# Kernel optimization log

Hardware: AMD Instinct MI355X
Metric: run time of the kernel (lower is better)

## Reference

```python
import jax, jax.numpy as jnp
import numpy as np
from functools import partial

B, EMB, H, V, T = 128, 512, 1024, 8192, 100
START_VALUE = 0


def setup_inputs() -> dict:
    key = jax.random.key(0)
    ks = jax.random.split(key, 8)
    s = 0.05
    return {
        "x": jax.random.normal(ks[0], (B, H), jnp.float32),
        "emb_table": jax.random.normal(ks[1], (V, EMB), jnp.float32) * s,
        "w_ih": jax.random.normal(ks[2], (3 * H, EMB), jnp.float32) * s,
        "w_hh": jax.random.normal(ks[3], (3 * H, H), jnp.float32) * s,
        "b_ih": jax.random.normal(ks[4], (3 * H,), jnp.float32) * s,
        "b_hh": jax.random.normal(ks[5], (3 * H,), jnp.float32) * s,
        "cls_w": jax.random.normal(ks[6], (V, H), jnp.float32) * s,
        "cls_b": jax.random.normal(ks[7], (V,), jnp.float32) * s,
    }


def _gru_cell(e, h, w_ih, w_hh, b_ih, b_hh):
    # PyTorch GRU cell math. e: [B,EMB], h: [B,H]
    gi = e @ w_ih.T + b_ih  # [B, 3H]
    gh = h @ w_hh.T + b_hh  # [B, 3H]
    i_r, i_z, i_n = jnp.split(gi, 3, axis=1)
    h_r, h_z, h_n = jnp.split(gh, 3, axis=1)
    r = jax.nn.sigmoid(i_r + h_r)
    z = jax.nn.sigmoid(i_z + h_z)
    n = jnp.tanh(i_n + r * h_n)
    return (1.0 - z) * n + z * h


def reference(x, emb_table, w_ih, w_hh, b_ih, b_hh, cls_w, cls_b):
    # start distribution: log_softmax of one-hot at START_VALUE
    start_val = jax.nn.log_softmax(
        jnp.zeros((V,), x.dtype).at[START_VALUE].set(1.0), axis=0
    )
    prev0 = jnp.broadcast_to(start_val, (B, V))

    def step(carry, _):
        h, prev_logp = carry
        idx = jnp.argmax(prev_logp, axis=1)          # [B]
        e = emb_table[idx]                           # [B, EMB]
        h_new = _gru_cell(e, h, w_ih, w_hh, b_ih, b_hh)
        logp = jax.nn.log_softmax(h_new @ cls_w.T + cls_b, axis=1)  # [B, V]
        return (h_new, logp), logp

    _, outs = jax.lax.scan(step, (x, prev0), None, length=T - 1)
    outs = jnp.transpose(outs, (1, 0, 2))            # [B, T-1, V]
    return jnp.concatenate([prev0[:, None, :], outs], axis=1)  # [B, T, V]
```

## Files before the change

kernel.cpp:

```cpp
#include <hip/hip_runtime.h>
#include <stdint.h>


#define Bb   128
#define EMBd 512
#define Hd   1024
#define Vd   8192
#define Td   100
#define HPB  524288

typedef __attribute__((ext_vector_type(8))) _Float16 half8;
typedef __attribute__((ext_vector_type(4))) float f32x4;
typedef unsigned long long ull;

#define LOSCALE 2048.0f
#define LOINV   (1.0f/2048.0f)

#define WAITV(N) do { asm volatile("s_waitcnt vmcnt(" #N ")" ::: "memory"); \
                      __builtin_amdgcn_sched_barrier(0); } while (0)
#define WAITL    do { asm volatile("s_waitcnt lgkmcnt(0)" ::: "memory");    \
                      __builtin_amdgcn_sched_barrier(0); } while (0)

__device__ __forceinline__ uint32_t fkey(float f) {
  uint32_t u = __float_as_uint(f);
  return (u & 0x80000000u) ? ~u : (u | 0x80000000u);
}
__device__ __forceinline__ ull umax64(ull a, ull b) { return a > b ? a : b; }

__device__ __forceinline__ void dma16(const void* g, void* l) {
  __builtin_amdgcn_global_load_lds((const uint32_t*)g, (uint32_t*)l, 16, 0, 0);
}
__device__ __forceinline__ void st16sc(void* p, half8 v) {
  f32x4 d = *(f32x4*)&v;
  asm volatile("global_store_dwordx4 %0, %1, off sc0 sc1"
               :: "v"(p), "v"(d) : "memory");
}
__device__ __forceinline__ ull sysld64(const ull* p) {
  return __hip_atomic_load((ull*)p, __ATOMIC_RELAXED, __HIP_MEMORY_SCOPE_SYSTEM);
}
__device__ __forceinline__ uint32_t ld32sys(uint32_t* p) {
  return __hip_atomic_load(p, __ATOMIC_RELAXED, __HIP_MEMORY_SCOPE_SYSTEM);
}
__device__ __forceinline__ void st32sys(uint32_t* p, uint32_t v) {
  __hip_atomic_store(p, v, __ATOMIC_RELAXED, __HIP_MEMORY_SCOPE_SYSTEM);
}
__device__ __forceinline__ uint32_t add32sys(uint32_t* p, uint32_t v) {
  return __hip_atomic_fetch_add(p, v, __ATOMIC_RELAXED, __HIP_MEMORY_SCOPE_SYSTEM);
}

__device__ __forceinline__ void cvt8(const float4 v0, const float4 v1,
                                     half8& hh, half8& ll) {
  float vv[8] = {v0.x, v0.y, v0.z, v0.w, v1.x, v1.y, v1.z, v1.w};
#pragma unroll
  for (int i = 0; i < 8; ++i) {
    _Float16 h = (_Float16)vv[i];
    hh[i] = h;
    ll[i] = (_Float16)((vv[i] - (float)h) * LOSCALE);
  }
}

__global__ void k_init(const float* __restrict__ x, float* __restrict__ hbuf0,
                       ull* __restrict__ amax, char* __restrict__ hpre0,
                       uint32_t* __restrict__ bar) {
  int tid = blockIdx.x * 256 + threadIdx.x;
  if (tid < Bb * Hd) hbuf0[tid] = x[tid];
  if (tid < Td * Bb) amax[tid] = (tid < Bb) ? 0xFFFFFFFFull : 0ull;
  if (tid >= 16384 && tid < 16640)
    bar[tid - 16384] = (tid - 16384 == 8) ? 128u : 0u;
  if (tid < 16384) {
    int b = tid & 127, sc = tid >> 7;
    int st = sc >> 2, c = sc & 3;
    const float* src = x + b * Hd + st * 32 + c * 8;
    float4 v0 = *(const float4*)src, v1 = *(const float4*)(src + 4);
    half8 hh, ll; cvt8(v0, v1, hh, ll);
    char* hp = hpre0 + st * 16384 + b * 128;
    *(half8*)(hp + ((c       ^ (b & 7))) * 16) = hh;
    *(half8*)(hp + (((c + 4) ^ (b & 7))) * 16) = ll;
  }
}

__global__ void k_prep_emb(const float* __restrict__ emb, char* __restrict__ embp) {
  int t = blockIdx.x * 256 + threadIdx.x;
  int row = t >> 6, rem = t & 63, st = rem >> 2, c = rem & 3;
  const float* src = emb + (size_t)row * EMBd + st * 32 + c * 8;
  float4 v0 = *(const float4*)src, v1 = *(const float4*)(src + 4);
  half8 hh, ll; cvt8(v0, v1, hh, ll);
  char* d = embp + (size_t)row * 2048 + st * 128;
  *(half8*)(d + c * 16) = hh;
  *(half8*)(d + (c + 4) * 16) = ll;
}

__global__ void k_prep_w(const float* __restrict__ w_ih, const float* __restrict__ w_hh,
                         char* __restrict__ wpre) {
  int bi = blockIdx.x;
  int st = bi % 12, t2 = bi / 12, q = t2 & 3, cg = t2 >> 2;
  int t = threadIdx.x; if (t >= 192) return;
  int r = t >> 2, c = t & 3;
  int g = r >> 4, bn = r & 15;
  int k0 = q * 384 + st * 32 + c * 8;
  const float* src = (k0 < 512)
    ? (w_ih + (size_t)(g * 1024 + cg * 16 + bn) * EMBd + k0)
    : (w_hh + (size_t)(g * 1024 + cg * 16 + bn) * Hd + (k0 - 512));
  float4 v0 = *(const float4*)src, v1 = *(const float4*)(src + 4);
  half8 hh, ll; cvt8(v0, v1, hh, ll);
  char* d = wpre + (size_t)bi * 6144 + r * 128;
  *(half8*)(d + ((c       ^ (r & 7))) * 16) = hh;
  *(half8*)(d + (((c + 4) ^ (r & 7))) * 16) = ll;
}

__global__ void k_prep_cls(const float* __restrict__ cls_w, char* __restrict__ clsp) {
  int b = blockIdx.x;
  int ct = b >> 5, st = b & 31;
  int t = threadIdx.x;
  int r = t >> 2, c = t & 3;
  const float* src = cls_w + (size_t)(ct * 64 + r) * Hd + st * 32 + c * 8;
  float4 v0 = *(const float4*)src, v1 = *(const float4*)(src + 4);
  half8 hh, ll; cvt8(v0, v1, hh, ll);
  char* d = clsp + (size_t)b * 8192 + r * 128;
  *(half8*)(d + ((c       ^ (r & 7))) * 16) = hh;
  *(half8*)(d + (((c + 4) ^ (r & 7))) * 16) = ll;
}

__global__ __launch_bounds__(256, 2) void k_prep_gi(
    const char* __restrict__ embp, const char* __restrict__ wpre,
    const float* __restrict__ b_ih, float* __restrict__ gi)
{
  const int cg = blockIdx.x, vh = blockIdx.y;
  const int tid = threadIdx.x, lane = tid & 63, w = tid >> 6;
  const int C = cg * 16;
  __shared__ __align__(16) char pA[4 * 8192];
  __shared__ __align__(16) char pB[4 * 6144];

  f32x4 accH[3], accL[3];
#pragma unroll
  for (int g = 0; g < 3; ++g) {
    accH[g] = (f32x4){0.f, 0.f, 0.f, 0.f};
    accL[g] = (f32x4){0.f, 0.f, 0.f, 0.f};
  }

  const int rr = lane >> 3, cc = lane & 7;
  const char* abase = embp + (size_t)(vh * 64 + w * 16 + rr) * 2048 + ((cc ^ rr) * 16);

  auto issue = [&](int st) {
    char* da = pA + (st & 3) * 8192 + w * 2048;
    const char* s0 = abase + st * 128;
    dma16(s0, da);
    dma16(s0 + 8 * 2048, da + 1024);
    const int wq = st / 12, wst = st - wq * 12;
    const char* sb = wpre + (size_t)((cg * 4 + wq) * 12 + wst) * 6144 + w * 1536 + lane * 16;
    char* db = pB + (st & 3) * 6144 + w * 1536;
    dma16(sb, db);
    if (lane < 32) dma16(sb + 1024, db + 1024);
  };

  const int l15 = lane & 15, qd = lane >> 4, r7 = l15 & 7;
  const int offAH = (w * 16 + l15) * 128 + ((qd)     ^ r7) * 16;
  const int offAL = (w * 16 + l15) * 128 + ((qd + 4) ^ r7) * 16;

  issue(0); issue(1); issue(2);
  WAITV(8);
  __builtin_amdgcn_s_barrier();

  for (int st = 0; st < 16; ++st) {
    const int bf = st & 3;
    half8 aH = *(half8*)&pA[bf * 8192 + offAH];
    half8 aL = *(half8*)&pA[bf * 8192 + offAL];
    if (st + 3 < 16) issue(st + 3);
#pragma unroll
    for (int g = 0; g < 3; ++g) {
      half8 bH = *(half8*)&pB[bf * 6144 + (g * 16 + l15) * 128 + ((qd)     ^ r7) * 16];
      half8 bL = *(half8*)&pB[bf * 6144 + (g * 16 + l15) * 128 + ((qd + 4) ^ r7) * 16];
      accH[g] = __builtin_amdgcn_mfma_f32_16x16x32_f16(aH, bH, accH[g], 0, 0, 0);
      accL[g] = __builtin_amdgcn_mfma_f32_16x16x32_f16(aH, bL, accL[g], 0, 0, 0);
      accL[g] = __builtin_amdgcn_mfma_f32_16x16x32_f16(aL, bH, accL[g], 0, 0, 0);
    }
    if (st < 15) {
      if (st <= 12)      { WAITV(8); }
      else if (st == 13) { WAITV(4); }
      else               { WAITV(0); }
      WAITL;
      __builtin_amdgcn_s_barrier();
    }
  }

  const int v0 = vh * 64 + w * 16 + qd * 4;
#pragma unroll
  for (int g = 0; g < 3; ++g) {
    float bi = b_ih[g * 1024 + C + l15];
#pragma unroll
    for (int i = 0; i < 4; ++i) {
      float val = accH[g][i] + accL[g][i] * LOINV + bi;
      gi[(size_t)(v0 + i) * 3072 + g * 1024 + C + l15] = val;
    }
  }
}

__global__ __launch_bounds__(256) void k_loop(
    const char* __restrict__ wpre, const char* __restrict__ clsp,
    const float* __restrict__ gi,
    const float* __restrict__ b_hh, const float* __restrict__ cls_b,
    float* __restrict__ hbuf, char* __restrict__ hpre,
    ull* __restrict__ amax, float* __restrict__ out,
    uint32_t* __restrict__ bar)
{
  const int wg = blockIdx.x;
  const int tid = threadIdx.x, lane = tid & 63, w = tid >> 6;
  __shared__ __align__(16) char smem[98304];

  if (tid == 0)
    (void)__hip_atomic_load(&bar[200], __ATOMIC_ACQUIRE, __HIP_MEMORY_SCOPE_AGENT);
  __syncthreads();

  uint32_t* gCnt   = &bar[0];
  uint32_t* hReady = &bar[1];
  uint32_t* aCnt   = &bar[8];

  const int l15 = lane & 15, qd = lane >> 4, r7 = l15 & 7;
  const int offA_H = (w * 16 + l15) * 128 + ((qd)     ^ r7) * 16;
  const int offA_L = (w * 16 + l15) * 128 + ((qd + 4) ^ r7) * 16;

  if (wg < 128) {
    const int cg = wg & 63, rh = wg >> 6;
    const int C = cg * 16;
    char* gA = smem;
    char* gB = smem + 32768;

    for (int s = 1; s < Td; ++s) {
      if (tid == 0)
        while (ld32sys(hReady) < (uint32_t)(s - 1)) __builtin_amdgcn_s_sleep(2);
      __syncthreads();

      const char* hsrc = hpre + (size_t)(s - 1) * HPB + rh * 8192 + w * 2048 + lane * 16;

      f32x4 accH[3], accL[3];
#pragma unroll
      for (int g = 0; g < 3; ++g) {
        accH[g] = (f32x4){0.f, 0.f, 0.f, 0.f};
        accL[g] = (f32x4){0.f, 0.f, 0.f, 0.f};
      }

      auto issue = [&](int st) {
        char* da = gA + (st & 3) * 8192 + w * 2048;
        const char* sa = hsrc + st * 16384;
        dma16(sa, da);
        dma16(sa + 1024, da + 1024);
        const int k0 = 512 + st * 32;
        const int wq = (k0 >= 1152) ? 3 : (k0 >= 768 ? 2 : 1);
        const int wst = (k0 - wq * 384) >> 5;
        const char* sb = wpre + (size_t)((cg * 4 + wq) * 12 + wst) * 6144 + w * 1536 + lane * 16;
        char* db = gB + (st & 3) * 6144 + w * 1536;
        dma16(sb, db);
        if (lane < 32) dma16(sb + 1024, db + 1024);
      };

      issue(0); issue(1); issue(2);
      WAITV(8);
      __builtin_amdgcn_s_barrier();

      for (int st = 0; st < 32; ++st) {
        const int bf = st & 3;
        half8 aH = *(half8*)&gA[bf * 8192 + offA_H];
        half8 aL = *(half8*)&gA[bf * 8192 + offA_L];
        if (st + 3 < 32) issue(st + 3);
#pragma unroll
        for (int g = 0; g < 3; ++g) {
          half8 bH = *(half8*)&gB[bf * 6144 + (g * 16 + l15) * 128 + ((qd)     ^ r7) * 16];
          half8 bL = *(half8*)&gB[bf * 6144 + (g * 16 + l15) * 128 + ((qd + 4) ^ r7) * 16];
          accH[g] = __builtin_amdgcn_mfma_f32_16x16x32_f16(aH, bH, accH[g], 0, 0, 0);
          accL[g] = __builtin_amdgcn_mfma_f32_16x16x32_f16(aH, bL, accL[g], 0, 0, 0);
          accL[g] = __builtin_amdgcn_mfma_f32_16x16x32_f16(aL, bH, accL[g], 0, 0, 0);
        }
        if (st < 31) {
          if (st <= 28)      { WAITV(8); }
          else if (st == 29) { WAITV(4); }
          else               { WAITV(0); }
          WAITL;
          __builtin_amdgcn_s_barrier();
        }
      }

      if (tid == 0)
        while (ld32sys(&aCnt[s - 1]) < 128u) __builtin_amdgcn_s_sleep(2);
      __syncthreads();

      const int j = C + l15;
      const float bh0 = b_hh[j], bh1 = b_hh[1024 + j], bh2 = b_hh[2048 + j];
      const float* hprev_f = hbuf + (size_t)((s - 1) & 1) * Bb * Hd;
      float* hnew_f = hbuf + (size_t)(s & 1) * Bb * Hd;
      const ull* amax_prev = amax + (size_t)(s - 1) * Bb;
      float outs[4];
#pragma unroll
      for (int i = 0; i < 4; ++i) {
        const int ri = rh * 64 + w * 16 + qd * 4 + i;
        const uint32_t idx = (~(uint32_t)sysld64(&amax_prev[ri])) & 8191u;
        const float* gp = gi + (size_t)idx * 3072 + j;
        float i_r = gp[0], i_z = gp[1024], i_n = gp[2048];
        float h_r = accH[0][i] + accL[0][i] * LOINV + bh0;
        float h_z = accH[1][i] + accL[1][i] * LOINV + bh1;
        float h_n = accH[2][i] + accL[2][i] * LOINV + bh2;
        float rr2 = 1.f / (1.f + expf(-(i_r + h_r)));
        float zz = 1.f / (1.f + expf(-(i_z + h_z)));
        float nn = tanhf(i_n + rr2 * h_n);
        float o = (1.f - zz) * nn + zz * hprev_f[ri * Hd + j];
        hnew_f[ri * Hd + j] = o;
        outs[i] = o;
      }
      __syncthreads();
      float* sT = (float*)smem;
#pragma unroll
      for (int i = 0; i < 4; ++i)
        sT[(w * 16 + qd * 4 + i) * 16 + l15] = outs[i];
      __syncthreads();
      if (tid < 128) {
        const int row = tid >> 1, half = tid & 1;
        const int b = rh * 64 + row;
        const float* srcp = sT + row * 16 + half * 8;
        half8 hh, ll;
#pragma unroll
        for (int e = 0; e < 8; ++e) {
          float o = srcp[e];
          _Float16 oh = (_Float16)o;
          hh[e] = oh;
          ll[e] = (_Float16)((o - (float)oh) * LOSCALE);
        }
        const int stp = C >> 5;
        const int chb = ((C & 31) >> 3) + half;
        char* hp = hpre + (size_t)s * HPB + stp * 16384 + b * 128;
        st16sc(hp + ((chb       ^ (b & 7))) * 16, hh);
        st16sc(hp + (((chb + 4) ^ (b & 7))) * 16, ll);
      }
      WAITV(0);
      __syncthreads();
      if (tid == 0) {
        uint32_t old = add32sys(gCnt, 1u);
        if (old + 1u == 128u * (uint32_t)s)
          st32sys(hReady, (uint32_t)s);
      }
    }
  } else {
    const int wgC = wg - 128;
    const int ct2 = wgC & 63, rt0 = wgC >> 6;
    const int r0c = rt0 * 64;
    char* cA = smem;
    char* cB = smem + 32768;
    const char* bb0 = clsp + (size_t)(2 * ct2)     * 262144 + w * 2048 + lane * 16;
    const char* bb1 = clsp + (size_t)(2 * ct2 + 1) * 262144 + w * 2048 + lane * 16;

    for (int s = 1; s < Td; ++s) {
      if (tid == 0)
        while (ld32sys(hReady) < (uint32_t)s) __builtin_amdgcn_s_sleep(2);
      __syncthreads();

      const char* asrc = hpre + (size_t)s * HPB + rt0 * 8192 + w * 2048 + lane * 16;

      f32x4 accH[8], accL[8];
#pragma unroll
      for (int i = 0; i < 8; ++i) {
        accH[i] = (f32x4){0.f, 0.f, 0.f, 0.f};
        accL[i] = (f32x4){0.f, 0.f, 0.f, 0.f};
      }

      auto issue = [&](int st) {
        char* da = cA + (st & 3) * 8192 + w * 2048;
        const char* sa = asrc + st * 16384;
        dma16(sa, da);
        dma16(sa + 1024, da + 1024);
        char* db = cB + (st & 3) * 16384 + w * 2048;
        const char* s0 = bb0 + st * 8192;
        dma16(s0, db);
        dma16(s0 + 1024, db + 1024);
        const char* s1 = bb1 + st * 8192;
        dma16(s1, db + 8192);
        dma16(s1 + 1024, db + 8192 + 1024);
      };

      issue(0); issue(1); issue(2);
      WAITV(12);
      __builtin_amdgcn_s_barrier();

      for (int st = 0; st < 32; ++st) {
        const int bf = st & 3;
        half8 aH = *(half8*)&cA[bf * 8192 + offA_H];
        half8 aL = *(half8*)&cA[bf * 8192 + offA_L];
        if (st + 3 < 32) issue(st + 3);
#pragma unroll
        for (int cf = 0; cf < 8; ++cf) {
          const int bo = bf * 16384 + (cf >> 2) * 8192 + ((cf & 3) * 16 + l15) * 128;
          half8 bH = *(half8*)&cB[bo + ((qd)     ^ r7) * 16];
          half8 bL = *(half8*)&cB[bo + ((qd + 4) ^ r7) * 16];
          accH[cf] = __builtin_amdgcn_mfma_f32_16x16x32_f16(aH, bH, accH[cf], 0, 0, 0);
          accL[cf] = __builtin_amdgcn_mfma_f32_16x16x32_f16(aH, bL, accL[cf], 0, 0, 0);
          accL[cf] = __builtin_amdgcn_mfma_f32_16x16x32_f16(aL, bH, accL[cf], 0, 0, 0);
        }
        if (st < 31) {
          if (st <= 28)      { WAITV(12); }
          else if (st == 29) { WAITV(6); }
          else               { WAITV(0); }
          WAITL;
          __builtin_amdgcn_s_barrier();
        }
      }

      float bsv[8];
#pragma unroll
      for (int cf = 0; cf < 8; ++cf)
        bsv[cf] = cls_b[(2 * ct2 + (cf >> 2)) * 64 + (cf & 3) * 16 + l15];
#pragma unroll
      for (int i = 0; i < 4; ++i) {
        const int brow = r0c + w * 16 + qd * 4 + i;
        float* orow = out + ((size_t)brow * Td + s) * Vd;
        ull best = 0ull;
#pragma unroll
        for (int cf = 0; cf < 8; ++cf) {
          const int v = (2 * ct2 + (cf >> 2)) * 64 + (cf & 3) * 16 + l15;
          float val = accH[cf][i] + accL[cf][i] * LOINV + bsv[cf];
          __builtin_nontemporal_store(val, &orow[v]);
          best = umax64(best, ((ull)fkey(val) << 32) | (uint32_t)(~(uint32_t)v));
        }
        best = umax64(best, __shfl_xor(best, 1));
        best = umax64(best, __shfl_xor(best, 2));
        best = umax64(best, __shfl_xor(best, 4));
        best = umax64(best, __shfl_xor(best, 8));
        if (l15 == 0) atomicMax(&amax[(size_t)s * Bb + brow], best);
      }
      WAITV(0);
      __syncthreads();
      if (tid == 0) add32sys(&aCnt[s], 1u);
    }
  }
}

__global__ void k_softmax(float* __restrict__ out,
                          const ull* __restrict__ amax) {
  int blk = blockIdx.x;
  int t = blk % Td, b = blk / Td;
  int tid = threadIdx.x;
  float* row = out + ((size_t)b * Td + t) * Vd;
  if (t == 0) {
    float lse0 = logf(expf(1.0f) + (float)(Vd - 1));
    for (int i = tid; i < Vd; i += 256) row[i] = ((i == 0) ? 1.0f : 0.0f) - lse0;
    return;
  }
  ull key = amax[t * Bb + b];
  uint32_t ku = (uint32_t)(key >> 32);
  uint32_t u = (ku & 0x80000000u) ? (ku & 0x7fffffffu) : ~ku;
  float m = __uint_as_float(u);
  float x[32];
  float ssum = 0.f;
#pragma unroll
  for (int i = 0; i < 32; ++i) {
    x[i] = row[tid + i * 256];
    ssum += expf(x[i] - m);
  }
  ssum += __shfl_xor(ssum, 1);
  ssum += __shfl_xor(ssum, 2);
  ssum += __shfl_xor(ssum, 4);
  ssum += __shfl_xor(ssum, 8);
  ssum += __shfl_xor(ssum, 16);
  ssum += __shfl_xor(ssum, 32);
  __shared__ float wsum[4];
  if ((tid & 63) == 0) wsum[tid >> 6] = ssum;
  __syncthreads();
  float lse = m + logf(wsum[0] + wsum[1] + wsum[2] + wsum[3]);
#pragma unroll
  for (int i = 0; i < 32; ++i) row[tid + i * 256] = x[i] - lse;
}

extern "C" void kernel_launch(void* const* d_in, const int* in_sizes, int n_in,
                              void* d_out, int out_size, void* d_ws, size_t ws_size,
                              hipStream_t stream) {
  const float* x     = (const float*)d_in[0];
  const float* emb   = (const float*)d_in[1];
  const float* w_ih  = (const float*)d_in[2];
  const float* w_hh  = (const float*)d_in[3];
  const float* b_ih  = (const float*)d_in[4];
  const float* b_hh  = (const float*)d_in[5];
  const float* cls_w = (const float*)d_in[6];
  const float* cls_b = (const float*)d_in[7];
  float* out = (float*)d_out;

  char* ws = (char*)d_ws;
  size_t o = 0;
  ull*      amax = (ull*)(ws + o);      o += (size_t)Td * Bb * 8;
  uint32_t* bar  = (uint32_t*)(ws + o); o += 1024;
  float*    hbuf = (float*)(ws + o);    o += (size_t)2 * Bb * Hd * 4;
  char*     hpre = ws + o;              o += (size_t)Td * HPB;
  char*     embp = ws + o;              o += (size_t)Vd * 2048;
  char*     wpre = ws + o;              o += (size_t)3072 * 6144;
  char*     clsp = ws + o;              o += (size_t)128 * 32 * 8192;
  float*    gi   = (float*)(ws + o);    o += (size_t)Vd * 3072 * 4;

  k_init<<<512, 256, 0, stream>>>(x, hbuf, amax, hpre, bar);
  k_prep_emb<<<2048, 256, 0, stream>>>(emb, embp);
  k_prep_w<<<3072, 256, 0, stream>>>(w_ih, w_hh, wpre);
  k_prep_cls<<<4096, 256, 0, stream>>>(cls_w, clsp);
  k_prep_gi<<<dim3(64, 128), 256, 0, stream>>>(embp, wpre, b_ih, gi);

  k_loop<<<256, 256, 0, stream>>>(wpre, clsp, gi, b_hh, cls_b,
                                  hbuf, hpre, amax, out, bar);

  k_softmax<<<12800, 256, 0, stream>>>(out, amax);
}
```

Before: 4.366 ms.

## Split persistent loop work across 512 workgroups with finer GRU and classifier tiles

The persistent loop kernel grows from 256 to 512 workgroups, and launch bounds now allow two per CU. GRU workgroups cover 32 rows instead of 64, with waves split by row half and gate set, and pass gate results through shared memory to the elementwise stage. Classifier workgroups cover 64 vocab columns instead of 128, and the barrier counts double to match. The aim is more CUs and more latency hiding per recurrent step, at the price of heavier cross-workgroup sync, more redundant A-tile loads and an uneven MFMA load between wave groups.

```diff
diff --git a/kernel.cpp b/kernel.cpp
--- a/kernel.cpp
+++ b/kernel.cpp
@@ -66,7 +66,7 @@
   if (tid < Bb * Hd) hbuf0[tid] = x[tid];
   if (tid < Td * Bb) amax[tid] = (tid < Bb) ? 0xFFFFFFFFull : 0ull;
   if (tid >= 16384 && tid < 16640)
-    bar[tid - 16384] = (tid - 16384 == 8) ? 128u : 0u;
+    bar[tid - 16384] = (tid - 16384 == 8) ? 256u : 0u;
   if (tid < 16384) {
     int b = tid & 127, sc = tid >> 7;
     int st = sc >> 2, c = sc & 3;
@@ -195,7 +195,7 @@
   }
 }
 
-__global__ __launch_bounds__(256) void k_loop(
+__global__ __launch_bounds__(256, 2) void k_loop(
     const char* __restrict__ wpre, const char* __restrict__ clsp,
     const float* __restrict__ gi,
     const float* __restrict__ b_hh, const float* __restrict__ cls_b,
@@ -205,7 +205,7 @@
 {
   const int wg = blockIdx.x;
   const int tid = threadIdx.x, lane = tid & 63, w = tid >> 6;
-  __shared__ __align__(16) char smem[98304];
+  __shared__ __align__(16) char smem[81920];
 
   if (tid == 0)
     (void)__hip_atomic_load(&bar[200], __ATOMIC_ACQUIRE, __HIP_MEMORY_SCOPE_AGENT);
@@ -216,34 +216,36 @@
   uint32_t* aCnt   = &bar[8];
 
   const int l15 = lane & 15, qd = lane >> 4, r7 = l15 & 7;
-  const int offA_H = (w * 16 + l15) * 128 + ((qd)     ^ r7) * 16;
-  const int offA_L = (w * 16 + l15) * 128 + ((qd + 4) ^ r7) * 16;
-
-  if (wg < 128) {
-    const int cg = wg & 63, rh = wg >> 6;
+
+  if (wg < 256) {
+    const int cg = wg & 63, rq = wg >> 6;
     const int C = cg * 16;
+    const int r2 = w & 1, gset = w >> 1;
     char* gA = smem;
-    char* gB = smem + 32768;
+    char* gB = smem + 16384;
+    float* sG = (float*)smem;
+    float* sT = (float*)(smem + 8192);
+
+    const int offGA_H = (r2 * 16 + l15) * 128 + ((qd)     ^ r7) * 16;
+    const int offGA_L = (r2 * 16 + l15) * 128 + ((qd + 4) ^ r7) * 16;
 
     for (int s = 1; s < Td; ++s) {
       if (tid == 0)
         while (ld32sys(hReady) < (uint32_t)(s - 1)) __builtin_amdgcn_s_sleep(2);
       __syncthreads();
 
-      const char* hsrc = hpre + (size_t)(s - 1) * HPB + rh * 8192 + w * 2048 + lane * 16;
-
-      f32x4 accH[3], accL[3];
-#pragma unroll
-      for (int g = 0; g < 3; ++g) {
+      const char* hsrc = hpre + (size_t)(s - 1) * HPB
+                         + (rq * 32 + w * 8) * 128 + lane * 16;
+
+      f32x4 accH[2], accL[2];
+#pragma unroll
+      for (int g = 0; g < 2; ++g) {
         accH[g] = (f32x4){0.f, 0.f, 0.f, 0.f};
         accL[g] = (f32x4){0.f, 0.f, 0.f, 0.f};
       }
 
       auto issue = [&](int st) {
-        char* da = gA + (st & 3) * 8192 + w * 2048;
-        const char* sa = hsrc + st * 16384;
-        dma16(sa, da);
-        dma16(sa + 1024, da + 1024);
+        dma16(hsrc + st * 16384, gA + (st & 3) * 4096 + w * 1024);
         const int k0 = 512 + st * 32;
         const int wq = (k0 >= 1152) ? 3 : (k0 >= 768 ? 2 : 1);
         const int wst = (k0 - wq * 384) >> 5;
@@ -254,25 +256,33 @@
       };
 
       issue(0); issue(1); issue(2);
-      WAITV(8);
+      WAITV(6);
       __builtin_amdgcn_s_barrier();
 
       for (int st = 0; st < 32; ++st) {
         const int bf = st & 3;
-        half8 aH = *(half8*)&gA[bf * 8192 + offA_H];
-        half8 aL = *(half8*)&gA[bf * 8192 + offA_L];
+        half8 aH = *(half8*)&gA[bf * 4096 + offGA_H];
+        half8 aL = *(half8*)&gA[bf * 4096 + offGA_L];
         if (st + 3 < 32) issue(st + 3);
-#pragma unroll
-        for (int g = 0; g < 3; ++g) {
-          half8 bH = *(half8*)&gB[bf * 6144 + (g * 16 + l15) * 128 + ((qd)     ^ r7) * 16];
-          half8 bL = *(half8*)&gB[bf * 6144 + (g * 16 + l15) * 128 + ((qd + 4) ^ r7) * 16];
-          accH[g] = __builtin_amdgcn_mfma_f32_16x16x32_f16(aH, bH, accH[g], 0, 0, 0);
-          accL[g] = __builtin_amdgcn_mfma_f32_16x16x32_f16(aH, bL, accL[g], 0, 0, 0);
-          accL[g] = __builtin_amdgcn_mfma_f32_16x16x32_f16(aL, bH, accL[g], 0, 0, 0);
+        if (gset == 0) {
+#pragma unroll
+          for (int g = 0; g < 2; ++g) {
+            half8 bH = *(half8*)&gB[bf * 6144 + (g * 16 + l15) * 128 + ((qd)     ^ r7) * 16];
+            half8 bL = *(half8*)&gB[bf * 6144 + (g * 16 + l15) * 128 + ((qd + 4) ^ r7) * 16];
+            accH[g] = __builtin_amdgcn_mfma_f32_16x16x32_f16(aH, bH, accH[g], 0, 0, 0);
+            accL[g] = __builtin_amdgcn_mfma_f32_16x16x32_f16(aH, bL, accL[g], 0, 0, 0);
+            accL[g] = __builtin_amdgcn_mfma_f32_16x16x32_f16(aL, bH, accL[g], 0, 0, 0);
+          }
+        } else {
+          half8 bH = *(half8*)&gB[bf * 6144 + (32 + l15) * 128 + ((qd)     ^ r7) * 16];
+          half8 bL = *(half8*)&gB[bf * 6144 + (32 + l15) * 128 + ((qd + 4) ^ r7) * 16];
+          accH[0] = __builtin_amdgcn_mfma_f32_16x16x32_f16(aH, bH, accH[0], 0, 0, 0);
+          accL[0] = __builtin_amdgcn_mfma_f32_16x16x32_f16(aH, bL, accL[0], 0, 0, 0);
+          accL[0] = __builtin_amdgcn_mfma_f32_16x16x32_f16(aL, bH, accL[0], 0, 0, 0);
         }
         if (st < 31) {
-          if (st <= 28)      { WAITV(8); }
-          else if (st == 29) { WAITV(4); }
+          if (st <= 28)      { WAITV(6); }
+          else if (st == 29) { WAITV(3); }
           else               { WAITV(0); }
           WAITL;
           __builtin_amdgcn_s_barrier();
@@ -280,40 +290,47 @@
       }
 
       if (tid == 0)
-        while (ld32sys(&aCnt[s - 1]) < 128u) __builtin_amdgcn_s_sleep(2);
-      __syncthreads();
-
-      const int j = C + l15;
-      const float bh0 = b_hh[j], bh1 = b_hh[1024 + j], bh2 = b_hh[2048 + j];
+        while (ld32sys(&aCnt[s - 1]) < 256u) __builtin_amdgcn_s_sleep(2);
+      __syncthreads();
+
+      if (gset == 0) {
+#pragma unroll
+        for (int g = 0; g < 2; ++g)
+#pragma unroll
+          for (int i = 0; i < 4; ++i)
+            sG[g * 512 + (r2 * 16 + qd * 4 + i) * 16 + l15] = accH[g][i] + accL[g][i] * LOINV;
+      } else {
+#pragma unroll
+        for (int i = 0; i < 4; ++i)
+          sG[1024 + (r2 * 16 + qd * 4 + i) * 16 + l15] = accH[0][i] + accL[0][i] * LOINV;
+      }
+      __syncthreads();
+
+      const ull* amax_prev = amax + (size_t)(s - 1) * Bb;
       const float* hprev_f = hbuf + (size_t)((s - 1) & 1) * Bb * Hd;
       float* hnew_f = hbuf + (size_t)(s & 1) * Bb * Hd;
-      const ull* amax_prev = amax + (size_t)(s - 1) * Bb;
-      float outs[4];
-#pragma unroll
-      for (int i = 0; i < 4; ++i) {
-        const int ri = rh * 64 + w * 16 + qd * 4 + i;
+#pragma unroll
+      for (int ee = 0; ee < 2; ++ee) {
+        const int e2 = tid + ee * 256;
+        const int r = e2 >> 4, c = e2 & 15;
+        const int ri = rq * 32 + r, j = C + c;
         const uint32_t idx = (~(uint32_t)sysld64(&amax_prev[ri])) & 8191u;
         const float* gp = gi + (size_t)idx * 3072 + j;
         float i_r = gp[0], i_z = gp[1024], i_n = gp[2048];
-        float h_r = accH[0][i] + accL[0][i] * LOINV + bh0;
-        float h_z = accH[1][i] + accL[1][i] * LOINV + bh1;
-        float h_n = accH[2][i] + accL[2][i] * LOINV + bh2;
+        float h_r = sG[e2]        + b_hh[j];
+        float h_z = sG[512 + e2]  + b_hh[1024 + j];
+        float h_n = sG[1024 + e2] + b_hh[2048 + j];
         float rr2 = 1.f / (1.f + expf(-(i_r + h_r)));
         float zz = 1.f / (1.f + expf(-(i_z + h_z)));
         float nn = tanhf(i_n + rr2 * h_n);
         float o = (1.f - zz) * nn + zz * hprev_f[ri * Hd + j];
         hnew_f[ri * Hd + j] = o;
-        outs[i] = o;
-      }
-      __syncthreads();
-      float* sT = (float*)smem;
-#pragma unroll
-      for (int i = 0; i < 4; ++i)
-        sT[(w * 16 + qd * 4 + i) * 16 + l15] = outs[i];
-      __syncthreads();
-      if (tid < 128) {
+        sT[e2] = o;
+      }
+      __syncthreads();
+      if (tid < 64) {
         const int row = tid >> 1, half = tid & 1;
-        const int b = rh * 64 + row;
+        const int b = rq * 32 + row;
         const float* srcp = sT + row * 16 + half * 8;
         half8 hh, ll;
 #pragma unroll
@@ -333,18 +350,20 @@
       __syncthreads();
       if (tid == 0) {
         uint32_t old = add32sys(gCnt, 1u);
-        if (old + 1u == 128u * (uint32_t)s)
+        if (old + 1u == 256u * (uint32_t)s)
           st32sys(hReady, (uint32_t)s);
       }
     }
   } else {
-    const int wgC = wg - 128;
-    const int ct2 = wgC & 63, rt0 = wgC >> 6;
-    const int r0c = rt0 * 64;
+    const int wgC = wg - 256;
+    const int ct = wgC & 127, rt0 = wgC >> 7;
+    const int r0c = rt0 * 64, c0c = ct * 64;
     char* cA = smem;
     char* cB = smem + 32768;
-    const char* bb0 = clsp + (size_t)(2 * ct2)     * 262144 + w * 2048 + lane * 16;
-    const char* bb1 = clsp + (size_t)(2 * ct2 + 1) * 262144 + w * 2048 + lane * 16;
+    const char* c_bsrc = clsp + (size_t)ct * 262144 + w * 2048 + lane * 16;
+
+    const int offA_H = (w * 16 + l15) * 128 + ((qd)     ^ r7) * 16;
+    const int offA_L = (w * 16 + l15) * 128 + ((qd + 4) ^ r7) * 16;
 
     for (int s = 1; s < Td; ++s) {
       if (tid == 0)
@@ -353,9 +372,9 @@
 
       const char* asrc = hpre + (size_t)s * HPB + rt0 * 8192 + w * 2048 + lane * 16;
 
-      f32x4 accH[8], accL[8];
-#pragma unroll
-      for (int i = 0; i < 8; ++i) {
+      f32x4 accH[4], accL[4];
+#pragma unroll
+      for (int i = 0; i < 4; ++i) {
         accH[i] = (f32x4){0.f, 0.f, 0.f, 0.f};
         accL[i] = (f32x4){0.f, 0.f, 0.f, 0.f};
       }
@@ -365,17 +384,14 @@
         const char* sa = asrc + st * 16384;
         dma16(sa, da);
         dma16(sa + 1024, da + 1024);
-        char* db = cB + (st & 3) * 16384 + w * 2048;
-        const char* s0 = bb0 + st * 8192;
-        dma16(s0, db);
-        dma16(s0 + 1024, db + 1024);
-        const char* s1 = bb1 + st * 8192;
-        dma16(s1, db + 8192);
-        dma16(s1 + 1024, db + 8192 + 1024);
+        char* db = cB + (st & 3) * 8192 + w * 2048;
+        const char* sb = c_bsrc + st * 8192;
+        dma16(sb, db);
+        dma16(sb + 1024, db + 1024);
       };
 
       issue(0); issue(1); issue(2);
-      WAITV(12);
+      WAITV(8);
       __builtin_amdgcn_s_barrier();
 
       for (int st = 0; st < 32; ++st) {
@@ -384,35 +400,33 @@
         half8 aL = *(half8*)&cA[bf * 8192 + offA_L];
         if (st + 3 < 32) issue(st + 3);
 #pragma unroll
-        for (int cf = 0; cf < 8; ++cf) {
-          const int bo = bf * 16384 + (cf >> 2) * 8192 + ((cf & 3) * 16 + l15) * 128;
-          half8 bH = *(half8*)&cB[bo + ((qd)     ^ r7) * 16];
-          half8 bL = *(half8*)&cB[bo + ((qd + 4) ^ r7) * 16];
+        for (int cf = 0; cf < 4; ++cf) {
+          half8 bH = *(half8*)&cB[bf * 8192 + (cf * 16 + l15) * 128 + ((qd)     ^ r7) * 16];
+          half8 bL = *(half8*)&cB[bf * 8192 + (cf * 16 + l15) * 128 + ((qd + 4) ^ r7) * 16];
           accH[cf] = __builtin_amdgcn_mfma_f32_16x16x32_f16(aH, bH, accH[cf], 0, 0, 0);
           accL[cf] = __builtin_amdgcn_mfma_f32_16x16x32_f16(aH, bL, accL[cf], 0, 0, 0);
           accL[cf] = __builtin_amdgcn_mfma_f32_16x16x32_f16(aL, bH, accL[cf], 0, 0, 0);
         }
         if (st < 31) {
-          if (st <= 28)      { WAITV(12); }
-          else if (st == 29) { WAITV(6); }
+          if (st <= 28)      { WAITV(8); }
+          else if (st == 29) { WAITV(4); }
           else               { WAITV(0); }
           WAITL;
           __builtin_amdgcn_s_barrier();
         }
       }
 
-      float bsv[8];
-#pragma unroll
-      for (int cf = 0; cf < 8; ++cf)
-        bsv[cf] = cls_b[(2 * ct2 + (cf >> 2)) * 64 + (cf & 3) * 16 + l15];
+      float bsv[4];
+#pragma unroll
+      for (int cf = 0; cf < 4; ++cf) bsv[cf] = cls_b[c0c + cf * 16 + l15];
 #pragma unroll
       for (int i = 0; i < 4; ++i) {
         const int brow = r0c + w * 16 + qd * 4 + i;
         float* orow = out + ((size_t)brow * Td + s) * Vd;
         ull best = 0ull;
 #pragma unroll
-        for (int cf = 0; cf < 8; ++cf) {
-          const int v = (2 * ct2 + (cf >> 2)) * 64 + (cf & 3) * 16 + l15;
+        for (int cf = 0; cf < 4; ++cf) {
+          const int v = c0c + cf * 16 + l15;
           float val = accH[cf][i] + accL[cf][i] * LOINV + bsv[cf];
           __builtin_nontemporal_store(val, &orow[v]);
           best = umax64(best, ((ull)fkey(val) << 32) | (uint32_t)(~(uint32_t)v));
@@ -496,7 +510,7 @@
   k_prep_cls<<<4096, 256, 0, stream>>>(cls_w, clsp);
   k_prep_gi<<<dim3(64, 128), 256, 0, stream>>>(embp, wpre, b_ih, gi);
 
-  k_loop<<<256, 256, 0, stream>>>(wpre, clsp, gi, b_hh, cls_b,
+  k_loop<<<512, 256, 0, stream>>>(wpre, clsp, gi, b_hh, cls_b,
                                   hbuf, hpre, amax, out, bar);
 
   k_softmax<<<12800, 256, 0, stream>>>(out, amax);
```

After: 4.504 ms. 3.1% more time.

## Deepen k_loop LDS DMA pipeline to six buffers with one barrier per stage

Applied to the files above, without the earlier changes.

The GRU-hidden and classifier GEMM loops in the persistent kernel grow their LDS ring from four to six stages and keep five DMA stages in flight instead of three. The vmcnt wait and barrier move to the top of each iteration, which removes the trailing lgkmcnt wait. The aim is to hide more global-load latency per step of this latency-bound recurrent loop. The cost is more shared memory (about 146 KB). The six-slot ring with five prefetched stages also relies on the top-of-loop barrier to keep overwrites of buffers still being read safe.

```diff
diff --git a/kernel.cpp b/kernel.cpp
--- a/kernel.cpp
+++ b/kernel.cpp
@@ -17,8 +17,6 @@
 #define LOINV   (1.0f/2048.0f)
 
 #define WAITV(N) do { asm volatile("s_waitcnt vmcnt(" #N ")" ::: "memory"); \
-                      __builtin_amdgcn_sched_barrier(0); } while (0)
-#define WAITL    do { asm volatile("s_waitcnt lgkmcnt(0)" ::: "memory");    \
                       __builtin_amdgcn_sched_barrier(0); } while (0)
 
 __device__ __forceinline__ uint32_t fkey(float f) {
@@ -178,7 +176,8 @@
       if (st <= 12)      { WAITV(8); }
       else if (st == 13) { WAITV(4); }
       else               { WAITV(0); }
-      WAITL;
+      asm volatile("s_waitcnt lgkmcnt(0)" ::: "memory");
+      __builtin_amdgcn_sched_barrier(0);
       __builtin_amdgcn_s_barrier();
     }
   }
@@ -205,7 +204,7 @@
 {
   const int wg = blockIdx.x;
   const int tid = threadIdx.x, lane = tid & 63, w = tid >> 6;
-  __shared__ __align__(16) char smem[98304];
+  __shared__ __align__(16) char smem[149504];
 
   if (tid == 0)
     (void)__hip_atomic_load(&bar[200], __ATOMIC_ACQUIRE, __HIP_MEMORY_SCOPE_AGENT);
@@ -223,7 +222,7 @@
     const int cg = wg & 63, rh = wg >> 6;
     const int C = cg * 16;
     char* gA = smem;
-    char* gB = smem + 32768;
+    char* gB = smem + 49152;
 
     for (int s = 1; s < Td; ++s) {
       if (tid == 0)
@@ -240,7 +239,8 @@
       }
 
       auto issue = [&](int st) {
-        char* da = gA + (st & 3) * 8192 + w * 2048;
+        const int bf = st % 6;
+        char* da = gA + bf * 8192 + w * 2048;
         const char* sa = hsrc + st * 16384;
         dma16(sa, da);
         dma16(sa + 1024, da + 1024);
@@ -248,20 +248,25 @@
         const int wq = (k0 >= 1152) ? 3 : (k0 >= 768 ? 2 : 1);
         const int wst = (k0 - wq * 384) >> 5;
         const char* sb = wpre + (size_t)((cg * 4 + wq) * 12 + wst) * 6144 + w * 1536 + lane * 16;
-        char* db = gB + (st & 3) * 6144 + w * 1536;
+        char* db = gB + bf * 6144 + w * 1536;
         dma16(sb, db);
         if (lane < 32) dma16(sb + 1024, db + 1024);
       };
 
-      issue(0); issue(1); issue(2);
-      WAITV(8);
-      __builtin_amdgcn_s_barrier();
+      issue(0); issue(1); issue(2); issue(3); issue(4);
 
       for (int st = 0; st < 32; ++st) {
-        const int bf = st & 3;
+        if (st <= 27)      { WAITV(12); }
+        else if (st == 28) { WAITV(9); }
+        else if (st == 29) { WAITV(6); }
+        else if (st == 30) { WAITV(3); }
+        else               { WAITV(0); }
+        __builtin_amdgcn_s_barrier();
+
+        const int bf = st % 6;
         half8 aH = *(half8*)&gA[bf * 8192 + offA_H];
         half8 aL = *(half8*)&gA[bf * 8192 + offA_L];
-        if (st + 3 < 32) issue(st + 3);
+        if (st + 5 < 32) issue(st + 5);
 #pragma unroll
         for (int g = 0; g < 3; ++g) {
           half8 bH = *(half8*)&gB[bf * 6144 + (g * 16 + l15) * 128 + ((qd)     ^ r7) * 16];
@@ -269,13 +274,6 @@
           accH[g] = __builtin_amdgcn_mfma_f32_16x16x32_f16(aH, bH, accH[g], 0, 0, 0);
           accL[g] = __builtin_amdgcn_mfma_f32_16x16x32_f16(aH, bL, accL[g], 0, 0, 0);
           accL[g] = __builtin_amdgcn_mfma_f32_16x16x32_f16(aL, bH, accL[g], 0, 0, 0);
-        }
-        if (st < 31) {
-          if (st <= 28)      { WAITV(8); }
-          else if (st == 29) { WAITV(4); }
-          else               { WAITV(0); }
-          WAITL;
-          __builtin_amdgcn_s_barrier();
         }
       }
 
@@ -342,7 +340,7 @@
     const int ct2 = wgC & 63, rt0 = wgC >> 6;
     const int r0c = rt0 * 64;
     char* cA = smem;
-    char* cB = smem + 32768;
+    char* cB = smem + 49152;
     const char* bb0 = clsp + (size_t)(2 * ct2)     * 262144 + w * 2048 + lane * 16;
     const char* bb1 = clsp + (size_t)(2 * ct2 + 1) * 262144 + w * 2048 + lane * 16;
 
@@ -361,11 +359,12 @@
       }
 
       auto issue = [&](int st) {
-        char* da = cA + (st & 3) * 8192 + w * 2048;
+        const int bf = st % 6;
+        char* da = cA + bf * 8192 + w * 2048;
         const char* sa = asrc + st * 16384;
         dma16(sa, da);
         dma16(sa + 1024, da + 1024);
-        char* db = cB + (st & 3) * 16384 + w * 2048;
+        char* db = cB + bf * 16384 + w * 2048;
         const char* s0 = bb0 + st * 8192;
         dma16(s0, db);
         dma16(s0 + 1024, db + 1024);
@@ -374,15 +373,20 @@
         dma16(s1 + 1024, db + 8192 + 1024);
       };
 
-      issue(0); issue(1); issue(2);
-      WAITV(12);
-      __builtin_amdgcn_s_barrier();
+      issue(0); issue(1); issue(2); issue(3); issue(4);
 
       for (int st = 0; st < 32; ++st) {
-        const int bf = st & 3;
+        if (st <= 27)      { WAITV(24); }
+        else if (st == 28) { WAITV(18); }
+        else if (st == 29) { WAITV(12); }
+        else if (st == 30) { WAITV(6); }
+        else               { WAITV(0); }
+        __builtin_amdgcn_s_barrier();
+
+        const int bf = st % 6;
         half8 aH = *(half8*)&cA[bf * 8192 + offA_H];
         half8 aL = *(half8*)&cA[bf * 8192 + offA_L];
-        if (st + 3 < 32) issue(st + 3);
+        if (st + 5 < 32) issue(st + 5);
 #pragma unroll
         for (int cf = 0; cf < 8; ++cf) {
           const int bo = bf * 16384 + (cf >> 2) * 8192 + ((cf & 3) * 16 + l15) * 128;
@@ -391,13 +395,6 @@
           accH[cf] = __builtin_amdgcn_mfma_f32_16x16x32_f16(aH, bH, accH[cf], 0, 0, 0);
           accL[cf] = __builtin_amdgcn_mfma_f32_16x16x32_f16(aH, bL, accL[cf], 0, 0, 0);
           accL[cf] = __builtin_amdgcn_mfma_f32_16x16x32_f16(aL, bH, accL[cf], 0, 0, 0);
-        }
-        if (st < 31) {
-          if (st <= 28)      { WAITV(12); }
-          else if (st == 29) { WAITV(6); }
-          else               { WAITV(0); }
-          WAITL;
-          __builtin_amdgcn_s_barrier();
         }
       }
 
```

New measurement: 4.524 ms. 3.6% more time.
